# Kernel optimization log

Hardware: AMD Instinct MI355X
Metric: run time of the kernel (lower is better)

The kernel has to match this reference:

```python
import jax, jax.numpy as jnp
import numpy as np

EMBED = 2048
HEADS = 16
KV_LEN = 4096
HEAD_DIM = EMBED // HEADS
LN_EPS = 1e-6


def _layernorm(x, scale, bias):
    m = jnp.mean(x, axis=-1, keepdims=True)
    v = jnp.var(x, axis=-1, keepdims=True)
    return (x - m) / jnp.sqrt(v + LN_EPS) * scale + bias


def setup_inputs() -> dict:
    key = jax.random.key(0)
    ks = jax.random.split(key, 12)
    d = EMBED
    s = 1.0 / np.sqrt(d)

    def W(k):
        return jax.random.normal(k, (d, d), jnp.float32) * s

    return {
        "x": jax.random.normal(ks[0], (d,), jnp.float32),
        "cache1": jax.random.normal(ks[1], (KV_LEN, HEADS, HEAD_DIM), jnp.float32),
        "cache2": jax.random.normal(ks[2], (KV_LEN, HEADS, HEAD_DIM), jnp.float32),
        "Wv": W(ks[3]), "bv": jnp.zeros((d,), jnp.float32),
        "Wq": W(ks[4]), "bq": jnp.zeros((d,), jnp.float32),
        "Wk": W(ks[5]), "bk": jnp.zeros((d,), jnp.float32),
        "Wo": W(ks[6]), "bo": jnp.zeros((d,), jnp.float32),
        "W1": W(ks[7]), "b1": jnp.zeros((d,), jnp.float32),
        "W2": W(ks[8]), "b2": jnp.zeros((d,), jnp.float32),
        "ln1_s": jnp.ones((d,), jnp.float32), "ln1_b": jnp.zeros((d,), jnp.float32),
        "ln2_s": jnp.ones((d,), jnp.float32), "ln2_b": jnp.zeros((d,), jnp.float32),
    }


def reference(x, cache1, cache2, Wv, bv, Wq, bq, Wk, bk, Wo, bo,
              W1, b1, W2, b2, ln1_s, ln1_b, ln2_s, ln2_b):
    H, hd = HEADS, HEAD_DIM
    # QKV projections for the single query token
    v_i = (x @ Wv + bv).reshape(1, H, hd)
    q_i = (x @ Wq + bq).reshape(H, hd)
    k_i = (x @ Wk + bk).reshape(1, H, hd)
    # roll caches: drop oldest, append newest
    v = jnp.concatenate((cache1[1:], v_i), axis=0)  # [K, H, hd]
    k = jnp.concatenate((cache2[1:], k_i), axis=0)
    # valid positions: any nonzero value in the v cache slot
    mask = jnp.any(v != 0, axis=(1, 2))  # [K]
    att = jnp.einsum('hd,khd->hk', q_i, k) / jnp.sqrt(jnp.float32(hd))
    att = jnp.where(mask, att, -jnp.inf)
    att = jax.nn.softmax(att, axis=-1)
    values = jnp.einsum('hk,khd->hd', att, v).reshape(EMBED)
    out = values @ Wo + bo
    # residual + LN, FFN (dropout deterministic -> no-op), residual + LN
    x1 = _layernorm(x + out, ln1_s, ln1_b)
    h = jax.nn.relu(x1 @ W1 + b1) @ W2 + b2
    x2 = _layernorm(x1 + h, ln2_s, ln2_b)
    return (x2, v, k)
```

## Files before the change

kernel.cpp:

```cpp
#include <hip/hip_runtime.h>
#include <hip/hip_bf16.h>
#include <stdint.h>

#define D    2048
#define H    16
#define HD   128
#define KV   4096
#define RSQRT_HD 0.08838834764831845f

typedef __attribute__((ext_vector_type(4))) float floatx4;


__global__ void k_matvec(const float* __restrict__ Wa, const float* __restrict__ Wb,
                         const float* __restrict__ Wc, const float* __restrict__ xin,
                         const float* __restrict__ prebias,
                         float* __restrict__ dst) {
    const float* W = (blockIdx.y == 0) ? Wa : (blockIdx.y == 1 ? Wb : Wc);
    float* d = dst + (size_t)blockIdx.y * D;
    int c0 = threadIdx.x * 4;
    int r0 = blockIdx.x * 32;
    floatx4 acc = {0.f, 0.f, 0.f, 0.f};
    for (int rb = 0; rb < 2; ++rb) {
        const float* Wp = W + (size_t)(r0 + rb * 16) * D + c0;
        floatx4 w[16];
#pragma unroll
        for (int i = 0; i < 16; ++i)
            w[i] = *reinterpret_cast<const floatx4*>(Wp + (size_t)i * D);
#pragma unroll
        for (int i = 0; i < 16; ++i) {
            int r = r0 + rb * 16 + i;
            float t = xin[r];
            if (prebias) t = fmaxf(t + prebias[r], 0.f);
            acc += t * w[i];
        }
    }
    atomicAdd(&d[c0 + 0], acc[0]);
    atomicAdd(&d[c0 + 1], acc[1]);
    atomicAdd(&d[c0 + 2], acc[2]);
    atomicAdd(&d[c0 + 3], acc[3]);
}

__global__ void k_roll_logits(const float* __restrict__ cache1,
                              const float* __restrict__ cache2,
                              const float* __restrict__ qs,
                              const float* __restrict__ bq,
                              const float* __restrict__ bk,
                              const float* __restrict__ bv,
                              float* __restrict__ outv,
                              float* __restrict__ outk,
                              float* __restrict__ att) {
    int wave = threadIdx.x >> 6;
    int lane = threadIdx.x & 63;
    int kk = blockIdx.x * 4 + wave;
    float pc[8];
    bool nz = false;
    float* vdst = outv + (size_t)kk * D;
    float* kdst = outk + (size_t)kk * D;

    if (kk < KV - 1) {
        const float* vsrc = cache1 + (size_t)(kk + 1) * D;
        const float* ksrc = cache2 + (size_t)(kk + 1) * D;
        floatx4 v[8], k[8];
#pragma unroll
        for (int c = 0; c < 8; ++c)
            v[c] = *reinterpret_cast<const floatx4*>(vsrc + c * 256 + lane * 4);
#pragma unroll
        for (int c = 0; c < 8; ++c)
            k[c] = *reinterpret_cast<const floatx4*>(ksrc + c * 256 + lane * 4);
#pragma unroll
        for (int c = 0; c < 8; ++c) {
            int e = c * 256 + lane * 4;
            *reinterpret_cast<floatx4*>(vdst + e) = v[c];
            *reinterpret_cast<floatx4*>(kdst + e) = k[c];
            nz = nz | (v[c][0] != 0.f) | (v[c][1] != 0.f) | (v[c][2] != 0.f) | (v[c][3] != 0.f);
            floatx4 q4 = *reinterpret_cast<const floatx4*>(qs + e);
            floatx4 b4 = *reinterpret_cast<const floatx4*>(bq + e);
            q4 += b4;
            pc[c] = q4[0]*k[c][0] + q4[1]*k[c][1] + q4[2]*k[c][2] + q4[3]*k[c][3];
        }
    } else {
#pragma unroll
        for (int c = 0; c < 8; ++c) {
            int e = c * 256 + lane * 4;
            floatx4 v4 = *reinterpret_cast<const floatx4*>(qs + 2 * D + e);
            floatx4 k4 = *reinterpret_cast<const floatx4*>(qs + D + e);
            v4 += *reinterpret_cast<const floatx4*>(bv + e);
            k4 += *reinterpret_cast<const floatx4*>(bk + e);
            *reinterpret_cast<floatx4*>(vdst + e) = v4;
            *reinterpret_cast<floatx4*>(kdst + e) = k4;
            nz = nz | (v4[0] != 0.f) | (v4[1] != 0.f) | (v4[2] != 0.f) | (v4[3] != 0.f);
            floatx4 q4 = *reinterpret_cast<const floatx4*>(qs + e);
            q4 += *reinterpret_cast<const floatx4*>(bq + e);
            pc[c] = q4[0]*k4[0] + q4[1]*k4[1] + q4[2]*k4[2] + q4[3]*k4[3];
        }
    }

    unsigned long long bal = __ballot(nz ? 1 : 0);
    bool anynz = (bal != 0ULL);

#pragma unroll
    for (int c = 0; c < 8; ++c) {
        float v = pc[c];
        v += __shfl_xor(v, 1);
        v += __shfl_xor(v, 2);
        v += __shfl_xor(v, 4);
        v += __shfl_xor(v, 8);
        v += __shfl_xor(v, 16);
        pc[c] = v;
    }
    if ((lane & 31) == 0) {
        int hi = lane >> 5;
#pragma unroll
        for (int c = 0; c < 8; ++c) {
            int h = c * 2 + hi;
            att[(size_t)h * KV + kk] = anynz ? pc[c] * RSQRT_HD : -INFINITY;
        }
    }
}

__global__ void k_softmax(float* __restrict__ att) {
    __shared__ float sred[4];
    int h = blockIdx.x;
    float* a = att + (size_t)h * KV;
    int t = threadIdx.x;
    float v[16];
    float m = -INFINITY;
#pragma unroll
    for (int i = 0; i < 16; ++i) {
        v[i] = a[i * 256 + t];
        m = fmaxf(m, v[i]);
    }
    for (int s = 32; s >= 1; s >>= 1) m = fmaxf(m, __shfl_xor(m, s));
    if ((t & 63) == 0) sred[t >> 6] = m;
    __syncthreads();
    m = fmaxf(fmaxf(sred[0], sred[1]), fmaxf(sred[2], sred[3]));
    __syncthreads();
    float sum = 0.f;
#pragma unroll
    for (int i = 0; i < 16; ++i) {
        v[i] = __expf(v[i] - m);
        sum += v[i];
    }
    for (int s = 32; s >= 1; s >>= 1) sum += __shfl_xor(sum, s);
    if ((t & 63) == 0) sred[t >> 6] = sum;
    __syncthreads();
    sum = sred[0] + sred[1] + sred[2] + sred[3];
    float inv = 1.0f / sum;
#pragma unroll
    for (int i = 0; i < 16; ++i) a[i * 256 + t] = v[i] * inv;
}

__global__ void k_av(const float* __restrict__ outv,
                     const float* __restrict__ att,
                     float* __restrict__ values) {
    int h = blockIdx.y;
    int c = blockIdx.x;
    int lane = threadIdx.x;
    int dg = (lane & 31) * 4;
    int ks = lane >> 5;
    floatx4 acc = {0.f, 0.f, 0.f, 0.f};
    int kk0 = c * 64;
#pragma unroll 8
    for (int i = 0; i < 32; ++i) {
        int kk = kk0 + i * 2 + ks;
        float a = att[(size_t)h * KV + kk];
        floatx4 v4 = *reinterpret_cast<const floatx4*>(outv + (size_t)kk * D + h * HD + dg);
        acc += a * v4;
    }
#pragma unroll
    for (int j = 0; j < 4; ++j) acc[j] += __shfl_xor(acc[j], 32);
    if (lane < 32) {
        float* p = values + h * HD + dg;
        atomicAdd(&p[0], acc[0]);
        atomicAdd(&p[1], acc[1]);
        atomicAdd(&p[2], acc[2]);
        atomicAdd(&p[3], acc[3]);
    }
}

__global__ void k_ln(const float* __restrict__ a, const float* __restrict__ b,
                     const float* __restrict__ bb,
                     const float* __restrict__ sc, const float* __restrict__ bi,
                     float* __restrict__ out) {
    __shared__ float sred[4];
    int t = threadIdx.x;
    float loc[8];
    float s = 0.f;
#pragma unroll
    for (int i = 0; i < 8; ++i) {
        int e = i * 256 + t;
        float v = a[e] + b[e] + bb[e];
        loc[i] = v;
        s += v;
    }
    for (int m = 32; m >= 1; m >>= 1) s += __shfl_xor(s, m);
    if ((t & 63) == 0) sred[t >> 6] = s;
    __syncthreads();
    float mean = (sred[0] + sred[1] + sred[2] + sred[3]) * (1.0f / D);
    __syncthreads();
    float vs = 0.f;
#pragma unroll
    for (int i = 0; i < 8; ++i) {
        float d = loc[i] - mean;
        vs += d * d;
    }
    for (int m = 32; m >= 1; m >>= 1) vs += __shfl_xor(vs, m);
    if ((t & 63) == 0) sred[t >> 6] = vs;
    __syncthreads();
    float var = (sred[0] + sred[1] + sred[2] + sred[3]) * (1.0f / D);
    float inv = 1.0f / sqrtf(var + 1e-6f);
#pragma unroll
    for (int i = 0; i < 8; ++i) {
        int e = i * 256 + t;
        out[e] = (loc[i] - mean) * inv * sc[e] + bi[e];
    }
}

extern "C" void kernel_launch(void* const* d_in, const int* in_sizes, int n_in,
                              void* d_out, int out_size, void* d_ws, size_t ws_size,
                              hipStream_t stream) {
    const float* x      = (const float*)d_in[0];
    const float* cache1 = (const float*)d_in[1];
    const float* cache2 = (const float*)d_in[2];
    const float* Wv     = (const float*)d_in[3];
    const float* bv     = (const float*)d_in[4];
    const float* Wq     = (const float*)d_in[5];
    const float* bq     = (const float*)d_in[6];
    const float* Wk     = (const float*)d_in[7];
    const float* bk     = (const float*)d_in[8];
    const float* Wo     = (const float*)d_in[9];
    const float* bo     = (const float*)d_in[10];
    const float* W1     = (const float*)d_in[11];
    const float* b1     = (const float*)d_in[12];
    const float* W2     = (const float*)d_in[13];
    const float* b2     = (const float*)d_in[14];
    const float* l1s    = (const float*)d_in[15];
    const float* l1b    = (const float*)d_in[16];
    const float* l2s    = (const float*)d_in[17];
    const float* l2b    = (const float*)d_in[18];

    float* out   = (float*)d_out;
    float* outx2 = out;
    float* outv  = out + D;
    float* outk  = out + D + (size_t)KV * D;

    float* w      = (float*)d_ws;
    float* qs     = w + 0;
    float* values = w + 6144;
    float* aout   = w + 8192;
    float* h1     = w + 10240;
    float* h2     = w + 12288;
    float* x1     = w + 14336;
    float* att    = w + 16384;

    hipMemsetAsync(w, 0, 14336 * sizeof(float), stream);

    k_matvec<<<dim3(64, 3), 512, 0, stream>>>(Wq, Wk, Wv, x, nullptr, qs);
    k_roll_logits<<<KV / 4, 256, 0, stream>>>(cache1, cache2, qs, bq, bk, bv, outv, outk, att);
    k_softmax<<<H, 256, 0, stream>>>(att);
    k_av<<<dim3(64, H), 64, 0, stream>>>(outv, att, values);
    k_matvec<<<dim3(64, 1), 512, 0, stream>>>(Wo, Wo, Wo, values, nullptr, aout);
    k_ln<<<1, 256, 0, stream>>>(x, aout, bo, l1s, l1b, x1);
    k_matvec<<<dim3(64, 1), 512, 0, stream>>>(W1, W1, W1, x1, nullptr, h1);
    k_matvec<<<dim3(64, 1), 512, 0, stream>>>(W2, W2, W2, h1, b1, h2);
    k_ln<<<1, 256, 0, stream>>>(x1, h2, b2, l2s, l2b, outx2);
}
```

Measured before the change: 292.4 us.

## Split fused roll+logits into memcpy, v-copy/mask, last-row and logits kernels

The single kernel that rolled both caches and computed logits is split apart. The K cache shift now goes through hipMemcpyAsync, and V is copied by a kernel that also writes a per-row mask. A one-block kernel writes the new last row, and a separate logits kernel rereads K from the output buffer. This likely aims to use the copy engine or a faster copy path, but it adds an extra 32 MB read of K plus three more launches.

```diff
diff --git a/kernel.cpp b/kernel.cpp
--- a/kernel.cpp
+++ b/kernel.cpp
@@ -40,64 +40,73 @@
     atomicAdd(&d[c0 + 3], acc[3]);
 }
 
-__global__ void k_roll_logits(const float* __restrict__ cache1,
-                              const float* __restrict__ cache2,
-                              const float* __restrict__ qs,
-                              const float* __restrict__ bq,
-                              const float* __restrict__ bk,
-                              const float* __restrict__ bv,
-                              float* __restrict__ outv,
-                              float* __restrict__ outk,
-                              float* __restrict__ att) {
+__global__ void k_copyv_mask(const float* __restrict__ cache1,
+                             float* __restrict__ outv,
+                             uint32_t* __restrict__ mask) {
     int wave = threadIdx.x >> 6;
     int lane = threadIdx.x & 63;
     int kk = blockIdx.x * 4 + wave;
+    if (kk >= KV - 1) return;
+    const float* src = cache1 + (size_t)(kk + 1) * D;
+    float* dst = outv + (size_t)kk * D;
+    floatx4 v[8];
+#pragma unroll
+    for (int c = 0; c < 8; ++c)
+        v[c] = *reinterpret_cast<const floatx4*>(src + c * 256 + lane * 4);
+    bool nz = false;
+#pragma unroll
+    for (int c = 0; c < 8; ++c) {
+        *reinterpret_cast<floatx4*>(dst + c * 256 + lane * 4) = v[c];
+        nz = nz | (v[c][0] != 0.f) | (v[c][1] != 0.f) | (v[c][2] != 0.f) | (v[c][3] != 0.f);
+    }
+    unsigned long long bal = __ballot(nz ? 1 : 0);
+    if (lane == 0) mask[kk] = (bal != 0ULL) ? 1u : 0u;
+}
+
+__global__ void k_lastrow(const float* __restrict__ qs,
+                          const float* __restrict__ bk,
+                          const float* __restrict__ bv,
+                          float* __restrict__ outv,
+                          float* __restrict__ outk,
+                          uint32_t* __restrict__ mask) {
+    __shared__ uint32_t snz;
+    int t = threadIdx.x;
+    if (t == 0) snz = 0;
+    __syncthreads();
+    bool nz = false;
+#pragma unroll
+    for (int i = 0; i < 8; ++i) {
+        int e = i * 256 + t;
+        float v = qs[2 * D + e] + bv[e];
+        float k = qs[D + e] + bk[e];
+        outv[(size_t)(KV - 1) * D + e] = v;
+        outk[(size_t)(KV - 1) * D + e] = k;
+        nz |= (v != 0.f);
+    }
+    if (__ballot(nz ? 1 : 0) != 0ULL) atomicOr(&snz, 1u);
+    __syncthreads();
+    if (t == 0) mask[KV - 1] = snz;
+}
+
+__global__ void k_logits(const float* __restrict__ outk,
+                         const float* __restrict__ qs,
+                         const float* __restrict__ bq,
+                         const uint32_t* __restrict__ mask,
+                         float* __restrict__ att) {
+    int wave = threadIdx.x >> 6;
+    int lane = threadIdx.x & 63;
+    int kk = blockIdx.x * 4 + wave;
+    const float* krow = outk + (size_t)kk * D;
     float pc[8];
-    bool nz = false;
-    float* vdst = outv + (size_t)kk * D;
-    float* kdst = outk + (size_t)kk * D;
-
-    if (kk < KV - 1) {
-        const float* vsrc = cache1 + (size_t)(kk + 1) * D;
-        const float* ksrc = cache2 + (size_t)(kk + 1) * D;
-        floatx4 v[8], k[8];
-#pragma unroll
-        for (int c = 0; c < 8; ++c)
-            v[c] = *reinterpret_cast<const floatx4*>(vsrc + c * 256 + lane * 4);
-#pragma unroll
-        for (int c = 0; c < 8; ++c)
-            k[c] = *reinterpret_cast<const floatx4*>(ksrc + c * 256 + lane * 4);
-#pragma unroll
-        for (int c = 0; c < 8; ++c) {
-            int e = c * 256 + lane * 4;
-            *reinterpret_cast<floatx4*>(vdst + e) = v[c];
-            *reinterpret_cast<floatx4*>(kdst + e) = k[c];
-            nz = nz | (v[c][0] != 0.f) | (v[c][1] != 0.f) | (v[c][2] != 0.f) | (v[c][3] != 0.f);
-            floatx4 q4 = *reinterpret_cast<const floatx4*>(qs + e);
-            floatx4 b4 = *reinterpret_cast<const floatx4*>(bq + e);
-            q4 += b4;
-            pc[c] = q4[0]*k[c][0] + q4[1]*k[c][1] + q4[2]*k[c][2] + q4[3]*k[c][3];
-        }
-    } else {
-#pragma unroll
-        for (int c = 0; c < 8; ++c) {
-            int e = c * 256 + lane * 4;
-            floatx4 v4 = *reinterpret_cast<const floatx4*>(qs + 2 * D + e);
-            floatx4 k4 = *reinterpret_cast<const floatx4*>(qs + D + e);
-            v4 += *reinterpret_cast<const floatx4*>(bv + e);
-            k4 += *reinterpret_cast<const floatx4*>(bk + e);
-            *reinterpret_cast<floatx4*>(vdst + e) = v4;
-            *reinterpret_cast<floatx4*>(kdst + e) = k4;
-            nz = nz | (v4[0] != 0.f) | (v4[1] != 0.f) | (v4[2] != 0.f) | (v4[3] != 0.f);
-            floatx4 q4 = *reinterpret_cast<const floatx4*>(qs + e);
-            q4 += *reinterpret_cast<const floatx4*>(bq + e);
-            pc[c] = q4[0]*k4[0] + q4[1]*k4[1] + q4[2]*k4[2] + q4[3]*k4[3];
-        }
-    }
-
-    unsigned long long bal = __ballot(nz ? 1 : 0);
-    bool anynz = (bal != 0ULL);
-
+#pragma unroll
+    for (int c = 0; c < 8; ++c) {
+        int e = c * 256 + lane * 4;
+        floatx4 k4 = *reinterpret_cast<const floatx4*>(krow + e);
+        floatx4 q4 = *reinterpret_cast<const floatx4*>(qs + e);
+        q4 += *reinterpret_cast<const floatx4*>(bq + e);
+        pc[c] = q4[0]*k4[0] + q4[1]*k4[1] + q4[2]*k4[2] + q4[3]*k4[3];
+    }
+    bool ok = (mask[kk] != 0u);
 #pragma unroll
     for (int c = 0; c < 8; ++c) {
         float v = pc[c];
@@ -113,7 +122,7 @@
 #pragma unroll
         for (int c = 0; c < 8; ++c) {
             int h = c * 2 + hi;
-            att[(size_t)h * KV + kk] = anynz ? pc[c] * RSQRT_HD : -INFINITY;
+            att[(size_t)h * KV + kk] = ok ? pc[c] * RSQRT_HD : -INFINITY;
         }
     }
 }
@@ -244,21 +253,29 @@
     float* outv  = out + D;
     float* outk  = out + D + (size_t)KV * D;
 
-    float* w      = (float*)d_ws;
-    float* qs     = w + 0;
-    float* values = w + 6144;
-    float* aout   = w + 8192;
-    float* h1     = w + 10240;
-    float* h2     = w + 12288;
-    float* x1     = w + 14336;
-    float* att    = w + 16384;
+    float* w        = (float*)d_ws;
+    float* qs       = w + 0;
+    float* values   = w + 6144;
+    float* aout     = w + 8192;
+    float* h1       = w + 10240;
+    float* h2       = w + 12288;
+    float* x1       = w + 14336;
+    float* att      = w + 16384;
+    uint32_t* mask  = (uint32_t*)(w + 81920);
 
     hipMemsetAsync(w, 0, 14336 * sizeof(float), stream);
 
     k_matvec<<<dim3(64, 3), 512, 0, stream>>>(Wq, Wk, Wv, x, nullptr, qs);
-    k_roll_logits<<<KV / 4, 256, 0, stream>>>(cache1, cache2, qs, bq, bk, bv, outv, outk, att);
+
+    hipMemcpyAsync(outk, cache2 + D, (size_t)(KV - 1) * D * sizeof(float),
+                   hipMemcpyDeviceToDevice, stream);
+    k_copyv_mask<<<KV / 4, 256, 0, stream>>>(cache1, outv, mask);
+    k_lastrow<<<1, 256, 0, stream>>>(qs, bk, bv, outv, outk, mask);
+
+    k_logits<<<KV / 4, 256, 0, stream>>>(outk, qs, bq, mask, att);
     k_softmax<<<H, 256, 0, stream>>>(att);
     k_av<<<dim3(64, H), 64, 0, stream>>>(outv, att, values);
+
     k_matvec<<<dim3(64, 1), 512, 0, stream>>>(Wo, Wo, Wo, values, nullptr, aout);
     k_ln<<<1, 256, 0, stream>>>(x, aout, bo, l1s, l1b, x1);
     k_matvec<<<dim3(64, 1), 512, 0, stream>>>(W1, W1, W1, x1, nullptr, h1);
```

New measurement: 303.6 us. 1.04x slower.
